# Optimization experiments

Measured on AMD Instinct MI355X. Metric: run time of the kernel, lower is better.

## Reference

```python
import jax, jax.numpy as jnp
import numpy as np

B, T, H, NH, L, V, FF = 2, 1024, 1024, 16, 6, 8192, 4096
D = H // NH
EPS = 1e-5


def _ln(x, g, b):
    mu = jnp.mean(x, axis=-1, keepdims=True)
    var = jnp.mean(jnp.square(x - mu), axis=-1, keepdims=True)
    return (x - mu) * jax.lax.rsqrt(var + EPS) * g + b


def setup_inputs() -> dict:
    key = jax.random.key(0)
    ks = jax.random.split(key, 12)
    s = 1.0 / np.sqrt(H)
    return {
        "x": jax.random.randint(ks[0], (B, T), 0, V),
        "tok_emb": jax.random.normal(ks[1], (V, H), jnp.float32) * s,
        "pos_emb": jax.random.normal(ks[2], (1, T, H), jnp.float32) * s,
        "Wq": jax.random.normal(ks[3], (L, H, H), jnp.float32) * s,
        "bq": jnp.zeros((L, H), jnp.float32),
        "Wk": jax.random.normal(ks[4], (L, H, H), jnp.float32) * s,
        "bk": jnp.zeros((L, H), jnp.float32),
        "Wv": jax.random.normal(ks[5], (L, H, H), jnp.float32) * s,
        "bv": jnp.zeros((L, H), jnp.float32),
        "Wo": jax.random.normal(ks[6], (L, H, H), jnp.float32) * s,
        "bo": jnp.zeros((L, H), jnp.float32),
        "W1": jax.random.normal(ks[7], (L, H, FF), jnp.float32) * s,
        "b1": jnp.zeros((L, FF), jnp.float32),
        "W2": jax.random.normal(ks[8], (L, FF, H), jnp.float32) * (1.0 / np.sqrt(FF)),
        "b2": jnp.zeros((L, H), jnp.float32),
        "ln1_g": jnp.ones((L, H), jnp.float32),
        "ln1_b": jnp.zeros((L, H), jnp.float32),
        "ln2_g": jnp.ones((L, H), jnp.float32),
        "ln2_b": jnp.zeros((L, H), jnp.float32),
        "lnf_g": jnp.ones((H,), jnp.float32),
        "lnf_b": jnp.zeros((H,), jnp.float32),
        "headW": jax.random.normal(ks[9], (H, V), jnp.float32) * s,
        "headb": jnp.zeros((V,), jnp.float32),
    }


def _transformer(x, tok_emb, pos_emb, Wq, bq, Wk, bk, Wv, bv, Wo, bo,
                 W1, b1, W2, b2, ln1_g, ln1_b, ln2_g, ln2_b, lnf_g, lnf_b,
                 headW, headb):
    Tcur = x.shape[1]
    h = tok_emb[x] + pos_emb[:, :Tcur, :]            # [B,T,H]
    mask = jnp.tril(jnp.ones((Tcur, Tcur), bool))    # causal [T,T]
    scale = 1.0 / np.sqrt(D)

    def block(h, p):
        (wq, q_b, wk, k_b, wv, v_b, wo, o_b,
         w1, b1_, w2, b2_, g1, be1, g2, be2) = p
        q = (h @ wq + q_b).reshape(B, Tcur, NH, D)
        k = (h @ wk + k_b).reshape(B, Tcur, NH, D)
        v = (h @ wv + v_b).reshape(B, Tcur, NH, D)
        att = jnp.einsum('bqnd,bknd->bnqk', q, k) * scale
        att = jnp.where(mask, att, -jnp.inf)
        w = jax.nn.softmax(att, axis=-1)
        o = jnp.einsum('bnqk,bknd->bqnd', w, v).reshape(B, Tcur, H)
        h = _ln(h + (o @ wo + o_b), g1, be1)          # post-LN after attention
        m = jax.nn.gelu(h @ w1 + b1_, approximate=False) @ w2 + b2_
        h = _ln(h + m, g2, be2)                       # post-LN after MLP
        return h, None

    params = (Wq, bq, Wk, bk, Wv, bv, Wo, bo, W1, b1, W2, b2,
              ln1_g, ln1_b, ln2_g, ln2_b)
    h, _ = jax.lax.scan(block, h, params)
    h = _ln(h, lnf_g, lnf_b)
    return h @ headW + headb                          # [B,T,V]


def reference(x, tok_emb, pos_emb, Wq, bq, Wk, bk, Wv, bv, Wo, bo,
              W1, b1, W2, b2, ln1_g, ln1_b, ln2_g, ln2_b, lnf_g, lnf_b,
              headW, headb):
    return _transformer(x, tok_emb, pos_emb, Wq, bq, Wk, bk, Wv, bv, Wo, bo,
                        W1, b1, W2, b2, ln1_g, ln1_b, ln2_g, ln2_b,
                        lnf_g, lnf_b, headW, headb)
```

## Files before the change

kernel.cpp:

```cpp
#include <hip/hip_runtime.h>
#include <hip/hip_bf16.h>

#define DEV __device__ __forceinline__

typedef unsigned short u16;
typedef __attribute__((ext_vector_type(8))) short bf16x8;
typedef __attribute__((ext_vector_type(4))) float f32x4;

static constexpr int MB_ = 2;
static constexpr int T_  = 1024;
static constexpr int H_  = 1024;
static constexpr int NH_ = 16;
static constexpr int L_  = 6;
static constexpr int V_  = 8192;
static constexpr int FF_ = 4096;
static constexpr int M_  = MB_ * T_;
static constexpr int QKVN = 3 * H_;

DEV u16 f2bf(float x) {
  __hip_bfloat16 h = __float2bfloat16(x);
  return *reinterpret_cast<u16*>(&h);
}
DEV float bf2f(u16 v) {
  unsigned u = (unsigned)v << 16;
  float f;
  __builtin_memcpy(&f, &u, 4);
  return f;
}

__global__ __launch_bounds__(256) void embed_concat_kernel(
    const int* __restrict__ x, const float* __restrict__ tok,
    const float* __restrict__ pos, float* __restrict__ h, u16* __restrict__ hb,
    const float* __restrict__ bq, const float* __restrict__ bk,
    const float* __restrict__ bv, float* __restrict__ outb)
{
  int i = blockIdx.x;
  if (i < M_) {
    int t = threadIdx.x;
    int id = x[i];
    int tt = i & (T_ - 1);
    float4 a = *(const float4*)(tok + (size_t)id * H_ + t * 4);
    float4 b = *(const float4*)(pos + (size_t)tt * H_ + t * 4);
    float4 r = make_float4(a.x + b.x, a.y + b.y, a.z + b.z, a.w + b.w);
    *(float4*)(h + (size_t)i * H_ + t * 4) = r;
    ushort4 u = make_ushort4(f2bf(r.x), f2bf(r.y), f2bf(r.z), f2bf(r.w));
    *(ushort4*)(hb + (size_t)i * H_ + t * 4) = u;
  } else {
    int l = i - M_;
    for (int j = threadIdx.x; j < H_; j += 256) {
      outb[(size_t)l * QKVN + j]          = bq[(size_t)l * H_ + j];
      outb[(size_t)l * QKVN + H_ + j]     = bk[(size_t)l * H_ + j];
      outb[(size_t)l * QKVN + 2 * H_ + j] = bv[(size_t)l * H_ + j];
    }
  }
}

DEV void transpose_tile128s(float (*Ts)[65], const float* __restrict__ W,
                            u16* __restrict__ WT, int R, int C, int bx, int by)
{
  const int t = threadIdx.x;
  const int lr = t >> 4;
  const int lcq = (t & 15) * 4;
  #pragma unroll
  for (int si = 0; si < 2; ++si) {
    #pragma unroll
    for (int sj = 0; sj < 2; ++sj) {
      const int r0 = by * 128 + si * 64, c0 = bx * 128 + sj * 64;
      #pragma unroll
      for (int it = 0; it < 4; ++it) {
        int r = it * 16 + lr;
        float4 v = *(const float4*)(W + (size_t)(r0 + r) * C + c0 + lcq);
        Ts[r][lcq + 0] = v.x; Ts[r][lcq + 1] = v.y;
        Ts[r][lcq + 2] = v.z; Ts[r][lcq + 3] = v.w;
      }
      __syncthreads();
      #pragma unroll
      for (int it = 0; it < 4; ++it) {
        int n = it * 16 + lr;
        ushort4 u = make_ushort4(f2bf(Ts[lcq + 0][n]), f2bf(Ts[lcq + 1][n]),
                                 f2bf(Ts[lcq + 2][n]), f2bf(Ts[lcq + 3][n]));
        *(ushort4*)(WT + (size_t)(c0 + n) * R + r0 + lcq) = u;
      }
      __syncthreads();
    }
  }
}

DEV void transpose_layer_body(float (*Ts)[65], int t,
    const float* Wq, const float* Wk, const float* Wv, const float* Wo,
    const float* W1, const float* W2,
    u16* qkvT, u16* oT, u16* w1T, u16* w2T)
{
  if (t < 256) {
    int m = t >> 6, idx = t & 63, bx = idx & 7, by = idx >> 3;
    const float* W = (m == 0) ? Wq : (m == 1) ? Wk : (m == 2) ? Wv : Wo;
    u16* WT = (m == 3) ? oT : qkvT + (size_t)m * H_ * H_;
    transpose_tile128s(Ts, W, WT, H_, H_, bx, by);
  } else if (t < 512) {
    int idx = t - 256;
    transpose_tile128s(Ts, W1, w1T, H_, FF_, idx & 31, idx >> 5);
  } else {
    int idx = t - 512;
    transpose_tile128s(Ts, W2, w2T, FF_, H_, idx & 7, idx >> 3);
  }
}

__global__ __launch_bounds__(256) void transpose_layer_k(
    const float* __restrict__ Wq, const float* __restrict__ Wk,
    const float* __restrict__ Wv, const float* __restrict__ Wo,
    const float* __restrict__ W1, const float* __restrict__ W2,
    u16* qkvT, u16* oT, u16* w1T, u16* w2T)
{
  __shared__ float Ts[64][65];
  transpose_layer_body(Ts, blockIdx.x, Wq, Wk, Wv, Wo, W1, W2, qkvT, oT, w1T, w2T);
}


#define GLOAD_LDS16(g, l)                                              \
  __builtin_amdgcn_global_load_lds(                                    \
      (const __attribute__((address_space(1))) void*)(g),              \
      (__attribute__((address_space(3))) void*)(l), 16, 0, 0)

DEV void stage_t(const u16* __restrict__ G, int ldk, int r0g, int kofs,
                 u16* lds, int w, int lane)
{
  const int rl = ((lane >> 3) << 1) | ((lane >> 2) & 1);
  #pragma unroll
  for (int j = 0; j < 2; ++j) {
    const int row0 = w * 32 + j * 16;
    const int row = row0 + rl;
    const int c = (lane & 3) ^ (((row0 >> 1) + (lane >> 3)) & 3);
    const u16* g = G + (size_t)(r0g + row) * ldk + kofs + c * 8;
    GLOAD_LDS16(g, lds + row0 * 32);
  }
}

DEV bf16x8 frag3(const u16* lds, int rr, int ch) {
  return *(const bf16x8*)(lds + (rr >> 1) * 64 + (rr & 1) * 32 +
                          ((ch ^ ((rr >> 1) & 3)) * 8));
}

template<int N>
DEV void wait_vm_barrier() {
  asm volatile("s_waitcnt vmcnt(%0)" :: "n"(N) : "memory");
  __builtin_amdgcn_s_barrier();
}

DEV void comp3(const u16* As, const u16* Bs, f32x4 (&acc)[4][4],
               int wr, int wc, int lc, int lg)
{
  bf16x8 af[4], bv[4];
  #pragma unroll
  for (int mi = 0; mi < 4; ++mi)
    af[mi] = frag3(As, wr * 64 + mi * 16 + lc, lg);
  #pragma unroll
  for (int ni = 0; ni < 4; ++ni)
    bv[ni] = frag3(Bs, wc * 64 + ni * 16 + lc, lg);
  #pragma unroll
  for (int mi = 0; mi < 4; ++mi)
    #pragma unroll
    for (int ni = 0; ni < 4; ++ni)
      acc[mi][ni] = __builtin_amdgcn_mfma_f32_16x16x32_bf16(af[mi], bv[ni], acc[mi][ni], 0, 0, 0);
}

template<bool PARTIAL, bool DO_GELU, bool WF, bool WB>
DEV void gemm_body(u16* SMEM,
    const u16* __restrict__ A, const u16* __restrict__ BT,
    const float* __restrict__ bias, float* __restrict__ Cf,
    u16* __restrict__ Cb, u16* __restrict__ Pb,
    int N, int K, int Ksub, int lid, int nwgx, int nwgy, int zid)
{
  const int tid = threadIdx.x;
  const int lane = tid & 63, w = tid >> 6;
  const int wr = w >> 1, wc = w & 1;
  const int lc = lane & 15, lg = lane >> 4;

  const int nwg = nwgx * nwgy;
  const int q8 = nwg >> 3, r8s = nwg & 7;
  const int xcd = lid & 7, ord = lid >> 3;
  const int sid = (xcd < r8s ? xcd * (q8 + 1) : r8s * (q8 + 1) + (xcd - r8s) * q8) + ord;
  const int m0 = (sid % nwgy) * 128, n0 = (sid / nwgy) * 128;

  const int kb = zid * Ksub;
  const int NT = Ksub >> 5;

  f32x4 acc[4][4];
  #pragma unroll
  for (int i = 0; i < 4; ++i)
    #pragma unroll
    for (int j = 0; j < 4; ++j) {
      f32x4 z = {0.f, 0.f, 0.f, 0.f};
      acc[i][j] = z;
    }

  auto STG = [&](int t, int b) {
    stage_t(A,  K, m0, kb + t * 32, SMEM + b * 4096, w, lane);
    stage_t(BT, K, n0, kb + t * 32, SMEM + 16384 + b * 4096, w, lane);
  };

  STG(0, 0);
  STG(1, 1);
  int t = 0;
  for (; t < NT - 2; ++t) {
    STG(t + 2, (t + 2) & 3);
    wait_vm_barrier<8>();
    comp3(SMEM + (t & 3) * 4096, SMEM + 16384 + (t & 3) * 4096, acc, wr, wc, lc, lg);
  }
  wait_vm_barrier<4>();
  comp3(SMEM + (t & 3) * 4096, SMEM + 16384 + (t & 3) * 4096, acc, wr, wc, lc, lg);
  ++t;
  wait_vm_barrier<0>();
  comp3(SMEM + (t & 3) * 4096, SMEM + 16384 + (t & 3) * 4096, acc, wr, wc, lc, lg);

  const size_t zofs = (size_t)zid * M_ * N;
  #pragma unroll
  for (int mi = 0; mi < 4; ++mi) {
    #pragma unroll
    for (int ni = 0; ni < 4; ++ni) {
      int gn = n0 + wc * 64 + ni * 16 + lc;
      float bvv = PARTIAL ? 0.f : bias[gn];
      #pragma unroll
      for (int r = 0; r < 4; ++r) {
        int gm = m0 + wr * 64 + mi * 16 + lg * 4 + r;
        float v = acc[mi][ni][r];
        if (PARTIAL) {
          Pb[zofs + (size_t)gm * N + gn] = f2bf(v);
        } else {
          v += bvv;
          if (DO_GELU) v = 0.5f * v * (1.f + erff(v * 0.70710678118654752f));
          if (WF) Cf[(size_t)gm * N + gn] = v;
          if (WB) Cb[(size_t)gm * N + gn] = f2bf(v);
        }
      }
    }
  }
}

template<bool PARTIAL, bool DO_GELU, bool WF, bool WB>
__global__ __launch_bounds__(256, 2) void gemm3(
    const u16* __restrict__ A, const u16* __restrict__ BT,
    const float* __restrict__ bias, float* __restrict__ Cf,
    u16* __restrict__ Cb, u16* __restrict__ Pb, int N, int K, int Ksub)
{
  __shared__ __align__(16) u16 SMEM[32768];
  gemm_body<PARTIAL, DO_GELU, WF, WB>(SMEM, A, BT, bias, Cf, Cb, Pb, N, K, Ksub,
      blockIdx.y * gridDim.x + blockIdx.x, gridDim.x, gridDim.y, blockIdx.z);
}

__global__ __launch_bounds__(256, 2) void gemmW1_fused(
    const u16* __restrict__ A, const u16* __restrict__ w1T,
    const float* __restrict__ bias, u16* __restrict__ m1,
    const float* nWq, const float* nWk, const float* nWv, const float* nWo,
    const float* nW1, const float* nW2,
    u16* nqkvT, u16* noT, u16* nw1T, u16* nw2T,
    const float* hW, u16* hT)
{
  __shared__ __align__(16) u16 SMEM[32768];
  const int id = blockIdx.x;
  if (id < 512) {
    gemm_body<false, true, false, true>(SMEM, A, w1T, bias, nullptr, m1, nullptr,
                                        FF_, H_, H_, id, 32, 16, 0);
  } else if (nWq) {
    float (*Ts)[65] = (float(*)[65])SMEM;
    transpose_layer_body(Ts, id - 512, nWq, nWk, nWv, nWo, nW1, nW2,
                         nqkvT, noT, nw1T, nw2T);
  } else {
    float (*Ts)[65] = (float(*)[65])SMEM;
    int idx = id - 512;
    transpose_tile128s(Ts, hW, hT, H_, V_, idx & 63, idx >> 6);
  }
}

__global__ __launch_bounds__(256) void ln2_kernel(
    const u16* __restrict__ Pb, int S,
    const float* __restrict__ bias,
    const float* __restrict__ g, const float* __restrict__ be,
    const float* __restrict__ gf, const float* __restrict__ bef,
    float* __restrict__ h, u16* __restrict__ hb)
{
  __shared__ float red[8];
  int row = blockIdx.x, t = threadIdx.x;
  int lane = t & 63, w = t >> 6;
  float4 v = *(const float4*)(h + (size_t)row * H_ + t * 4);
  float4 bb = *(const float4*)(bias + t * 4);
  v.x += bb.x; v.y += bb.y; v.z += bb.z; v.w += bb.w;
  for (int s0 = 0; s0 < S; ++s0) {
    ushort4 p = *(const ushort4*)(Pb + (size_t)s0 * M_ * H_ + (size_t)row * H_ + t * 4);
    v.x += bf2f(p.x); v.y += bf2f(p.y); v.z += bf2f(p.z); v.w += bf2f(p.w);
  }
  float s = v.x + v.y + v.z + v.w;
  float q = v.x * v.x + v.y * v.y + v.z * v.z + v.w * v.w;
  #pragma unroll
  for (int o = 1; o < 64; o <<= 1) { s += __shfl_xor(s, o); q += __shfl_xor(q, o); }
  if (lane == 0) { red[w] = s; red[4 + w] = q; }
  __syncthreads();
  float S1 = red[0] + red[1] + red[2] + red[3];
  float Q1 = red[4] + red[5] + red[6] + red[7];
  float mu  = S1 * (1.f / H_);
  float var = Q1 * (1.f / H_) - mu * mu;
  float inv = rsqrtf(var + 1e-5f);
  float4 gv = *(const float4*)(g  + t * 4);
  float4 bv = *(const float4*)(be + t * 4);
  float o0 = (v.x - mu) * inv * gv.x + bv.x;
  float o1 = (v.y - mu) * inv * gv.y + bv.y;
  float o2 = (v.z - mu) * inv * gv.z + bv.z;
  float o3 = (v.w - mu) * inv * gv.w + bv.w;
  if (gf == nullptr) {
    *(float4*)(h + (size_t)row * H_ + t * 4) = make_float4(o0, o1, o2, o3);
    ushort4 u = make_ushort4(f2bf(o0), f2bf(o1), f2bf(o2), f2bf(o3));
    *(ushort4*)(hb + (size_t)row * H_ + t * 4) = u;
  } else {
    float s2 = o0 + o1 + o2 + o3;
    float q2 = o0 * o0 + o1 * o1 + o2 * o2 + o3 * o3;
    #pragma unroll
    for (int o = 1; o < 64; o <<= 1) { s2 += __shfl_xor(s2, o); q2 += __shfl_xor(q2, o); }
    __syncthreads();
    if (lane == 0) { red[w] = s2; red[4 + w] = q2; }
    __syncthreads();
    float S2 = red[0] + red[1] + red[2] + red[3];
    float Q2 = red[4] + red[5] + red[6] + red[7];
    float mu2  = S2 * (1.f / H_);
    float var2 = Q2 * (1.f / H_) - mu2 * mu2;
    float inv2 = rsqrtf(var2 + 1e-5f);
    float4 gv2 = *(const float4*)(gf  + t * 4);
    float4 bv2 = *(const float4*)(bef + t * 4);
    ushort4 u = make_ushort4(f2bf((o0 - mu2) * inv2 * gv2.x + bv2.x),
                             f2bf((o1 - mu2) * inv2 * gv2.y + bv2.y),
                             f2bf((o2 - mu2) * inv2 * gv2.z + bv2.z),
                             f2bf((o3 - mu2) * inv2 * gv2.w + bv2.w));
    *(ushort4*)(hb + (size_t)row * H_ + t * 4) = u;
  }
}

__global__ __launch_bounds__(256) void attn_kernel(
    const u16* __restrict__ qkv, u16* __restrict__ Og)
{
  __shared__ __align__(16) u16 Ks[2][64][72];
  __shared__ __align__(16) u16 Vs[2][64][72];
  __shared__ __align__(16) u16 QPs[4][16][72];

  const int qb = gridDim.x - 1 - blockIdx.x;
  const int bh = blockIdx.y;
  const int b = bh >> 4, hh = bh & 15;
  const int q0 = qb * 64;
  const size_t base  = ((size_t)b * T_) * QKVN + (size_t)hh * 64;
  const size_t baseO = ((size_t)b * T_) * H_ + (size_t)hh * 64;

  const int tid = threadIdx.x;
  const int lane = tid & 63, w = tid >> 6;
  const int lc = lane & 15, lg = lane >> 4;

  const int r8 = tid >> 3, d8 = (tid & 7) << 3;
  const int vk = tid & 31, vd = (tid >> 5) << 3;

  u16* Qflat = &QPs[0][0][0];

  bf16x8 kr[2], vr[2];
  #pragma unroll
  for (int i = 0; i < 2; ++i) {
    kr[i] = *(const bf16x8*)(qkv + base + H_ + (size_t)(i * 32 + r8) * QKVN + d8);
    vr[i] = *(const bf16x8*)(qkv + base + 2 * H_ + (size_t)(i * 32 + vk) * QKVN + vd);
  }
  #pragma unroll
  for (int i = 0; i < 2; ++i)
    *(bf16x8*)(Qflat + (size_t)(i * 32 + r8) * 72 + d8) =
      *(const bf16x8*)(qkv + base + (size_t)(q0 + i * 32 + r8) * QKVN + d8);
  #pragma unroll
  for (int i = 0; i < 2; ++i) {
    *(bf16x8*)&Ks[0][i * 32 + r8][d8] = kr[i];
    #pragma unroll
    for (int j = 0; j < 8; ++j) Vs[0][vd + j][i * 32 + vk] = ((const u16*)&vr[i])[j];
  }
  __syncthreads();
  bf16x8 aq0 = *(const bf16x8*)(Qflat + (size_t)(w * 16 + lc) * 72 + lg * 8);
  bf16x8 aq1 = *(const bf16x8*)(Qflat + (size_t)(w * 16 + lc) * 72 + 32 + lg * 8);

  float m_r[4], l_r[4];
  f32x4 oa[4];
  #pragma unroll
  for (int i = 0; i < 4; ++i) {
    m_r[i] = -1e30f; l_r[i] = 0.f;
    f32x4 z = {0.f, 0.f, 0.f, 0.f};
    oa[i] = z;
  }
  const float sc2 = 0.125f * 1.4426950408889634f;

  for (int kv = 0; kv <= qb; ++kv) {
    const int cur = kv & 1, nxt = cur ^ 1;
    if (kv < qb) {
      #pragma unroll
      for (int i = 0; i < 2; ++i) {
        kr[i] = *(const bf16x8*)(qkv + base + H_ + (size_t)((kv + 1) * 64 + i * 32 + r8) * QKVN + d8);
        vr[i] = *(const bf16x8*)(qkv + base + 2 * H_ + (size_t)((kv + 1) * 64 + i * 32 + vk) * QKVN + vd);
      }
    }

    f32x4 sfr[4];
    #pragma unroll
    for (int ni = 0; ni < 4; ++ni) { f32x4 z = {0.f,0.f,0.f,0.f}; sfr[ni] = z; }
    __builtin_amdgcn_s_setprio(1);
    #pragma unroll
    for (int ni = 0; ni < 4; ++ni) {
      bf16x8 bk0 = *(const bf16x8*)&Ks[cur][ni * 16 + lc][lg * 8];
      bf16x8 bk1 = *(const bf16x8*)&Ks[cur][ni * 16 + lc][32 + lg * 8];
      sfr[ni] = __builtin_amdgcn_mfma_f32_16x16x32_bf16(aq0, bk0, sfr[ni], 0, 0, 0);
      sfr[ni] = __builtin_amdgcn_mfma_f32_16x16x32_bf16(aq1, bk1, sfr[ni], 0, 0, 0);
    }
    __builtin_amdgcn_s_setprio(0);
    if (kv == qb) {
      #pragma unroll
      for (int ni = 0; ni < 4; ++ni)
        #pragma unroll
        for (int r = 0; r < 4; ++r)
          if (ni * 16 + lc > w * 16 + lg * 4 + r) sfr[ni][r] = -1e30f;
    }
    #pragma unroll
    for (int r = 0; r < 4; ++r) {
      float pm = fmaxf(fmaxf(sfr[0][r], sfr[1][r]), fmaxf(sfr[2][r], sfr[3][r]));
      pm = fmaxf(pm, __shfl_xor(pm, 1));
      pm = fmaxf(pm, __shfl_xor(pm, 2));
      pm = fmaxf(pm, __shfl_xor(pm, 4));
      pm = fmaxf(pm, __shfl_xor(pm, 8));
      float mn = fmaxf(m_r[r], pm);
      float al = exp2f(sc2 * (m_r[r] - mn));
      m_r[r] = mn; l_r[r] *= al;
      #pragma unroll
      for (int f = 0; f < 4; ++f) oa[f][r] *= al;
      float rs = 0.f;
      #pragma unroll
      for (int ni = 0; ni < 4; ++ni) {
        float p = exp2f(sc2 * (sfr[ni][r] - mn));
        sfr[ni][r] = p; rs += p;
      }
      rs += __shfl_xor(rs, 1); rs += __shfl_xor(rs, 2);
      rs += __shfl_xor(rs, 4); rs += __shfl_xor(rs, 8);
      l_r[r] += rs;
    }
    #pragma unroll
    for (int ni = 0; ni < 4; ++ni)
      #pragma unroll
      for (int r = 0; r < 4; ++r)
        QPs[w][lg * 4 + r][ni * 16 + lc] = f2bf(sfr[ni][r]);
    bf16x8 ap0 = *(const bf16x8*)&QPs[w][lc][lg * 8];
    bf16x8 ap1 = *(const bf16x8*)&QPs[w][lc][32 + lg * 8];
    __builtin_amdgcn_s_setprio(1);
    #pragma unroll
    for (int f = 0; f < 4; ++f) {
      bf16x8 bv0 = *(const bf16x8*)&Vs[cur][f * 16 + lc][lg * 8];
      bf16x8 bv1 = *(const bf16x8*)&Vs[cur][f * 16 + lc][32 + lg * 8];
      oa[f] = __builtin_amdgcn_mfma_f32_16x16x32_bf16(ap0, bv0, oa[f], 0, 0, 0);
      oa[f] = __builtin_amdgcn_mfma_f32_16x16x32_bf16(ap1, bv1, oa[f], 0, 0, 0);
    }
    __builtin_amdgcn_s_setprio(0);

    if (kv < qb) {
      #pragma unroll
      for (int i = 0; i < 2; ++i) {
        *(bf16x8*)&Ks[nxt][i * 32 + r8][d8] = kr[i];
        #pragma unroll
        for (int j = 0; j < 8; ++j) Vs[nxt][vd + j][i * 32 + vk] = ((const u16*)&vr[i])[j];
      }
      __syncthreads();
    }
  }

  #pragma unroll
  for (int r = 0; r < 4; ++r) {
    float inv = 1.f / l_r[r];
    int grow = q0 + w * 16 + lg * 4 + r;
    #pragma unroll
    for (int f = 0; f < 4; ++f)
      Og[baseO + (size_t)grow * H_ + f * 16 + lc] = f2bf(oa[f][r] * inv);
  }
}

extern "C" void kernel_launch(void* const* d_in, const int* in_sizes, int n_in,
                              void* d_out, int out_size, void* d_ws, size_t ws_size,
                              hipStream_t stream)
{
  const int*   x    = (const int*)  d_in[0];
  const float* tok  = (const float*)d_in[1];
  const float* pos  = (const float*)d_in[2];
  const float* Wq   = (const float*)d_in[3];
  const float* bq   = (const float*)d_in[4];
  const float* Wk   = (const float*)d_in[5];
  const float* bk   = (const float*)d_in[6];
  const float* Wv   = (const float*)d_in[7];
  const float* bv   = (const float*)d_in[8];
  const float* Wo   = (const float*)d_in[9];
  const float* bo   = (const float*)d_in[10];
  const float* W1   = (const float*)d_in[11];
  const float* b1   = (const float*)d_in[12];
  const float* W2   = (const float*)d_in[13];
  const float* b2   = (const float*)d_in[14];
  const float* g1   = (const float*)d_in[15];
  const float* be1  = (const float*)d_in[16];
  const float* g2   = (const float*)d_in[17];
  const float* be2  = (const float*)d_in[18];
  const float* gf   = (const float*)d_in[19];
  const float* bef  = (const float*)d_in[20];
  const float* hW   = (const float*)d_in[21];
  const float* hbias= (const float*)d_in[22];
  float* out = (float*)d_out;

  char* wsp = (char*)d_ws;
  size_t off = 0;
  auto alloc = [&](size_t bytes) -> void* {
    void* p = wsp + off;
    off += (bytes + 255) & ~(size_t)255;
    return p;
  };
  float* h    = (float*)alloc((size_t)M_ * H_ * 4);
  u16*   hb   = (u16*)  alloc((size_t)M_ * H_ * 2);
  u16*   qkv  = (u16*)  alloc((size_t)M_ * QKVN * 2);
  u16*   ob_  = (u16*)  alloc((size_t)M_ * H_ * 2);
  u16*   m1   = (u16*)  alloc((size_t)M_ * FF_ * 2);
  u16*   Pb   = (u16*)  alloc((size_t)4 * M_ * H_ * 2);
  u16*   hT   = (u16*)  alloc((size_t)V_ * H_ * 2);
  u16*   qkvT = (u16*)  alloc((size_t)QKVN * H_ * 2);
  u16*   oT   = (u16*)  alloc((size_t)H_ * H_ * 2);
  u16*   w1Tb = (u16*)  alloc((size_t)2 * H_ * FF_ * 2);
  u16*   w2Tb = (u16*)  alloc((size_t)2 * FF_ * H_ * 2);
  float* bqkv = (float*)alloc((size_t)L_ * QKVN * 4);
  (void)in_sizes; (void)n_in; (void)out_size; (void)ws_size;

  auto w1T = [&](int l) { return w1Tb + (size_t)(l & 1) * H_ * FF_; };
  auto w2T = [&](int l) { return w2Tb + (size_t)(l & 1) * FF_ * H_; };

  embed_concat_kernel<<<M_ + L_, 256, 0, stream>>>(x, tok, pos, h, hb,
                                                   bq, bk, bv, bqkv);
  transpose_layer_k<<<768, 256, 0, stream>>>(
      Wq, Wk, Wv, Wo, W1, W2, qkvT, oT, w1T(0), w2T(0));

  for (int l = 0; l < L_; ++l) {
    gemm3<false, false, false, true><<<dim3(QKVN / 128, M_ / 128, 1), 256, 0, stream>>>(
        hb, qkvT, bqkv + (size_t)l * QKVN, nullptr, qkv, nullptr, QKVN, H_, H_);
    attn_kernel<<<dim3(T_ / 64, MB_ * NH_), 256, 0, stream>>>(qkv, ob_);
    gemm3<true, false, false, false><<<dim3(H_ / 128, M_ / 128, 4), 256, 0, stream>>>(
        ob_, oT, nullptr, nullptr, nullptr, Pb, H_, H_, H_ / 4);
    ln2_kernel<<<M_, 256, 0, stream>>>(Pb, 4, bo + l * H_, g1 + l * H_, be1 + l * H_,
                                       nullptr, nullptr, h, hb);
    if (l + 1 < L_) {
      int nl = l + 1;
      gemmW1_fused<<<512 + 768, 256, 0, stream>>>(
          hb, w1T(l), b1 + (size_t)l * FF_, m1,
          Wq + (size_t)nl * H_ * H_, Wk + (size_t)nl * H_ * H_,
          Wv + (size_t)nl * H_ * H_, Wo + (size_t)nl * H_ * H_,
          W1 + (size_t)nl * H_ * FF_, W2 + (size_t)nl * FF_ * H_,
          qkvT, oT, w1T(nl), w2T(nl), nullptr, nullptr);
    } else {
      gemmW1_fused<<<512 + 512, 256, 0, stream>>>(
          hb, w1T(l), b1 + (size_t)l * FF_, m1,
          nullptr, nullptr, nullptr, nullptr, nullptr, nullptr,
          nullptr, nullptr, nullptr, nullptr, hW, hT);
    }
    gemm3<true, false, false, false><<<dim3(H_ / 128, M_ / 128, 4), 256, 0, stream>>>(
        m1, w2T(l), nullptr, nullptr, nullptr, Pb, H_, FF_, FF_ / 4);
    if (l + 1 < L_) {
      ln2_kernel<<<M_, 256, 0, stream>>>(Pb, 4, b2 + l * H_, g2 + l * H_, be2 + l * H_,
                                         nullptr, nullptr, h, hb);
    } else {
      ln2_kernel<<<M_, 256, 0, stream>>>(Pb, 4, b2 + l * H_, g2 + l * H_, be2 + l * H_,
                                         gf, bef, h, hb);
    }
  }

  gemm3<false, false, true, false><<<dim3(V_ / 128, M_ / 128, 1), 256, 0, stream>>>(
      hb, hT, hbias, out, nullptr, nullptr, V_, H_, H_);
}
```

Measured before the change: 1.006 ms.

## Widen GEMM tiles to 128x256 with 512-thread workgroups and dynamic LDS

Replaces the 128x128, 256-thread GEMM kernel with a 128x256 tile computed by 8 waves (2x4 wave grid), staging B with twice as many rows per k-step into a larger 4-stage ring held in 96KB of dynamic shared memory. The goal is more reuse of each A tile per staged byte and fewer workgroups per GEMM. The fused W1 kernel and its weight-transpose side work now run at 512 threads, with the upper half of threads idle during transposes. Risks: one workgroup per CU lowers occupancy, and the grids get smaller, so some GEMMs (for example the split-K ones with 128 workgroups) may underfill the GPU.

New measurement: 1.020 ms. No clear change (+1.4%).

```diff
diff --git a/kernel.cpp b/kernel.cpp
--- a/kernel.cpp
+++ b/kernel.cpp
@@ -16,6 +16,7 @@
 static constexpr int FF_ = 4096;
 static constexpr int M_  = MB_ * T_;
 static constexpr int QKVN = 3 * H_;
+static constexpr size_t GLDS = 98304;
 
 DEV u16 f2bf(float x) {
   __hip_bfloat16 h = __float2bfloat16(x);
@@ -59,27 +60,32 @@
                             u16* __restrict__ WT, int R, int C, int bx, int by)
 {
   const int t = threadIdx.x;
-  const int lr = t >> 4;
+  const bool act = t < 256;
+  const int lr = (t & 255) >> 4;
   const int lcq = (t & 15) * 4;
   #pragma unroll
   for (int si = 0; si < 2; ++si) {
     #pragma unroll
     for (int sj = 0; sj < 2; ++sj) {
       const int r0 = by * 128 + si * 64, c0 = bx * 128 + sj * 64;
-      #pragma unroll
-      for (int it = 0; it < 4; ++it) {
-        int r = it * 16 + lr;
-        float4 v = *(const float4*)(W + (size_t)(r0 + r) * C + c0 + lcq);
-        Ts[r][lcq + 0] = v.x; Ts[r][lcq + 1] = v.y;
-        Ts[r][lcq + 2] = v.z; Ts[r][lcq + 3] = v.w;
+      if (act) {
+        #pragma unroll
+        for (int it = 0; it < 4; ++it) {
+          int r = it * 16 + lr;
+          float4 v = *(const float4*)(W + (size_t)(r0 + r) * C + c0 + lcq);
+          Ts[r][lcq + 0] = v.x; Ts[r][lcq + 1] = v.y;
+          Ts[r][lcq + 2] = v.z; Ts[r][lcq + 3] = v.w;
+        }
       }
       __syncthreads();
-      #pragma unroll
-      for (int it = 0; it < 4; ++it) {
-        int n = it * 16 + lr;
-        ushort4 u = make_ushort4(f2bf(Ts[lcq + 0][n]), f2bf(Ts[lcq + 1][n]),
-                                 f2bf(Ts[lcq + 2][n]), f2bf(Ts[lcq + 3][n]));
-        *(ushort4*)(WT + (size_t)(c0 + n) * R + r0 + lcq) = u;
+      if (act) {
+        #pragma unroll
+        for (int it = 0; it < 4; ++it) {
+          int n = it * 16 + lr;
+          ushort4 u = make_ushort4(f2bf(Ts[lcq + 0][n]), f2bf(Ts[lcq + 1][n]),
+                                   f2bf(Ts[lcq + 2][n]), f2bf(Ts[lcq + 3][n]));
+          *(ushort4*)(WT + (size_t)(c0 + n) * R + r0 + lcq) = u;
+        }
       }
       __syncthreads();
     }
@@ -121,18 +127,14 @@
       (const __attribute__((address_space(1))) void*)(g),              \
       (__attribute__((address_space(3))) void*)(l), 16, 0, 0)
 
-DEV void stage_t(const u16* __restrict__ G, int ldk, int r0g, int kofs,
-                 u16* lds, int w, int lane)
+DEV void stage_rows16(const u16* __restrict__ G, int ldk, int r0g, int row0,
+                      int kofs, u16* lds, int lane)
 {
   const int rl = ((lane >> 3) << 1) | ((lane >> 2) & 1);
-  #pragma unroll
-  for (int j = 0; j < 2; ++j) {
-    const int row0 = w * 32 + j * 16;
-    const int row = row0 + rl;
-    const int c = (lane & 3) ^ (((row0 >> 1) + (lane >> 3)) & 3);
-    const u16* g = G + (size_t)(r0g + row) * ldk + kofs + c * 8;
-    GLOAD_LDS16(g, lds + row0 * 32);
-  }
+  const int row = row0 + rl;
+  const int c = (lane & 3) ^ (((row0 >> 1) + (lane >> 3)) & 3);
+  const u16* g = G + (size_t)(r0g + row) * ldk + kofs + c * 8;
+  GLOAD_LDS16(g, lds + row0 * 32);
 }
 
 DEV bf16x8 frag3(const u16* lds, int rr, int ch) {
@@ -146,16 +148,16 @@
   __builtin_amdgcn_s_barrier();
 }
 
-DEV void comp3(const u16* As, const u16* Bs, f32x4 (&acc)[4][4],
-               int wr, int wc, int lc, int lg)
+DEV void comp8(const u16* As, const u16* Bs, f32x4 (&acc)[4][4],
+               int wm, int wn, int lc, int lg)
 {
   bf16x8 af[4], bv[4];
   #pragma unroll
   for (int mi = 0; mi < 4; ++mi)
-    af[mi] = frag3(As, wr * 64 + mi * 16 + lc, lg);
+    af[mi] = frag3(As, wm * 64 + mi * 16 + lc, lg);
   #pragma unroll
   for (int ni = 0; ni < 4; ++ni)
-    bv[ni] = frag3(Bs, wc * 64 + ni * 16 + lc, lg);
+    bv[ni] = frag3(Bs, wn * 64 + ni * 16 + lc, lg);
   #pragma unroll
   for (int mi = 0; mi < 4; ++mi)
     #pragma unroll
@@ -164,7 +166,7 @@
 }
 
 template<bool PARTIAL, bool DO_GELU, bool WF, bool WB>
-DEV void gemm_body(u16* SMEM,
+DEV void gemm8_body(u16* SMEM,
     const u16* __restrict__ A, const u16* __restrict__ BT,
     const float* __restrict__ bias, float* __restrict__ Cf,
     u16* __restrict__ Cb, u16* __restrict__ Pb,
@@ -172,14 +174,14 @@
 {
   const int tid = threadIdx.x;
   const int lane = tid & 63, w = tid >> 6;
-  const int wr = w >> 1, wc = w & 1;
+  const int wm = w >> 2, wn = w & 3;
   const int lc = lane & 15, lg = lane >> 4;
 
   const int nwg = nwgx * nwgy;
   const int q8 = nwg >> 3, r8s = nwg & 7;
   const int xcd = lid & 7, ord = lid >> 3;
   const int sid = (xcd < r8s ? xcd * (q8 + 1) : r8s * (q8 + 1) + (xcd - r8s) * q8) + ord;
-  const int m0 = (sid % nwgy) * 128, n0 = (sid / nwgy) * 128;
+  const int m0 = (sid % nwgy) * 128, n0 = (sid / nwgy) * 256;
 
   const int kb = zid * Ksub;
   const int NT = Ksub >> 5;
@@ -194,8 +196,9 @@
     }
 
   auto STG = [&](int t, int b) {
-    stage_t(A,  K, m0, kb + t * 32, SMEM + b * 4096, w, lane);
-    stage_t(BT, K, n0, kb + t * 32, SMEM + 16384 + b * 4096, w, lane);
+    stage_rows16(A,  K, m0, w * 16,      kb + t * 32, SMEM + b * 4096, lane);
+    stage_rows16(BT, K, n0, w * 32,      kb + t * 32, SMEM + 16384 + b * 8192, lane);
+    stage_rows16(BT, K, n0, w * 32 + 16, kb + t * 32, SMEM + 16384 + b * 8192, lane);
   };
 
   STG(0, 0);
@@ -203,25 +206,25 @@
   int t = 0;
   for (; t < NT - 2; ++t) {
     STG(t + 2, (t + 2) & 3);
-    wait_vm_barrier<8>();
-    comp3(SMEM + (t & 3) * 4096, SMEM + 16384 + (t & 3) * 4096, acc, wr, wc, lc, lg);
-  }
-  wait_vm_barrier<4>();
-  comp3(SMEM + (t & 3) * 4096, SMEM + 16384 + (t & 3) * 4096, acc, wr, wc, lc, lg);
+    wait_vm_barrier<6>();
+    comp8(SMEM + (t & 3) * 4096, SMEM + 16384 + (t & 3) * 8192, acc, wm, wn, lc, lg);
+  }
+  wait_vm_barrier<3>();
+  comp8(SMEM + (t & 3) * 4096, SMEM + 16384 + (t & 3) * 8192, acc, wm, wn, lc, lg);
   ++t;
   wait_vm_barrier<0>();
-  comp3(SMEM + (t & 3) * 4096, SMEM + 16384 + (t & 3) * 4096, acc, wr, wc, lc, lg);
+  comp8(SMEM + (t & 3) * 4096, SMEM + 16384 + (t & 3) * 8192, acc, wm, wn, lc, lg);
 
   const size_t zofs = (size_t)zid * M_ * N;
   #pragma unroll
   for (int mi = 0; mi < 4; ++mi) {
     #pragma unroll
     for (int ni = 0; ni < 4; ++ni) {
-      int gn = n0 + wc * 64 + ni * 16 + lc;
+      int gn = n0 + wn * 64 + ni * 16 + lc;
       float bvv = PARTIAL ? 0.f : bias[gn];
       #pragma unroll
       for (int r = 0; r < 4; ++r) {
-        int gm = m0 + wr * 64 + mi * 16 + lg * 4 + r;
+        int gm = m0 + wm * 64 + mi * 16 + lg * 4 + r;
         float v = acc[mi][ni][r];
         if (PARTIAL) {
           Pb[zofs + (size_t)gm * N + gn] = f2bf(v);
@@ -237,17 +240,17 @@
 }
 
 template<bool PARTIAL, bool DO_GELU, bool WF, bool WB>
-__global__ __launch_bounds__(256, 2) void gemm3(
+__global__ __launch_bounds__(512, 1) void gemm8(
     const u16* __restrict__ A, const u16* __restrict__ BT,
     const float* __restrict__ bias, float* __restrict__ Cf,
     u16* __restrict__ Cb, u16* __restrict__ Pb, int N, int K, int Ksub)
 {
-  __shared__ __align__(16) u16 SMEM[32768];
-  gemm_body<PARTIAL, DO_GELU, WF, WB>(SMEM, A, BT, bias, Cf, Cb, Pb, N, K, Ksub,
+  extern __shared__ __align__(16) u16 SMEM[];
+  gemm8_body<PARTIAL, DO_GELU, WF, WB>(SMEM, A, BT, bias, Cf, Cb, Pb, N, K, Ksub,
       blockIdx.y * gridDim.x + blockIdx.x, gridDim.x, gridDim.y, blockIdx.z);
 }
 
-__global__ __launch_bounds__(256, 2) void gemmW1_fused(
+__global__ __launch_bounds__(512, 1) void gemmW1_fused(
     const u16* __restrict__ A, const u16* __restrict__ w1T,
     const float* __restrict__ bias, u16* __restrict__ m1,
     const float* nWq, const float* nWk, const float* nWv, const float* nWo,
@@ -255,18 +258,18 @@
     u16* nqkvT, u16* noT, u16* nw1T, u16* nw2T,
     const float* hW, u16* hT)
 {
-  __shared__ __align__(16) u16 SMEM[32768];
+  extern __shared__ __align__(16) u16 SMEM[];
   const int id = blockIdx.x;
-  if (id < 512) {
-    gemm_body<false, true, false, true>(SMEM, A, w1T, bias, nullptr, m1, nullptr,
-                                        FF_, H_, H_, id, 32, 16, 0);
+  if (id < 256) {
+    gemm8_body<false, true, false, true>(SMEM, A, w1T, bias, nullptr, m1, nullptr,
+                                         FF_, H_, H_, id, 16, 16, 0);
   } else if (nWq) {
     float (*Ts)[65] = (float(*)[65])SMEM;
-    transpose_layer_body(Ts, id - 512, nWq, nWk, nWv, nWo, nW1, nW2,
+    transpose_layer_body(Ts, id - 256, nWq, nWk, nWv, nWo, nW1, nW2,
                          nqkvT, noT, nw1T, nw2T);
   } else {
     float (*Ts)[65] = (float(*)[65])SMEM;
-    int idx = id - 512;
+    int idx = id - 256;
     transpose_tile128s(Ts, hW, hT, H_, V_, idx & 63, idx >> 6);
   }
 }
@@ -533,28 +536,28 @@
       Wq, Wk, Wv, Wo, W1, W2, qkvT, oT, w1T(0), w2T(0));
 
   for (int l = 0; l < L_; ++l) {
-    gemm3<false, false, false, true><<<dim3(QKVN / 128, M_ / 128, 1), 256, 0, stream>>>(
+    gemm8<false, false, false, true><<<dim3(QKVN / 256, M_ / 128, 1), 512, GLDS, stream>>>(
         hb, qkvT, bqkv + (size_t)l * QKVN, nullptr, qkv, nullptr, QKVN, H_, H_);
     attn_kernel<<<dim3(T_ / 64, MB_ * NH_), 256, 0, stream>>>(qkv, ob_);
-    gemm3<true, false, false, false><<<dim3(H_ / 128, M_ / 128, 4), 256, 0, stream>>>(
+    gemm8<true, false, false, false><<<dim3(H_ / 256, M_ / 128, 4), 512, GLDS, stream>>>(
         ob_, oT, nullptr, nullptr, nullptr, Pb, H_, H_, H_ / 4);
     ln2_kernel<<<M_, 256, 0, stream>>>(Pb, 4, bo + l * H_, g1 + l * H_, be1 + l * H_,
                                        nullptr, nullptr, h, hb);
     if (l + 1 < L_) {
       int nl = l + 1;
-      gemmW1_fused<<<512 + 768, 256, 0, stream>>>(
+      gemmW1_fused<<<256 + 768, 512, GLDS, stream>>>(
           hb, w1T(l), b1 + (size_t)l * FF_, m1,
           Wq + (size_t)nl * H_ * H_, Wk + (size_t)nl * H_ * H_,
           Wv + (size_t)nl * H_ * H_, Wo + (size_t)nl * H_ * H_,
           W1 + (size_t)nl * H_ * FF_, W2 + (size_t)nl * FF_ * H_,
           qkvT, oT, w1T(nl), w2T(nl), nullptr, nullptr);
     } else {
-      gemmW1_fused<<<512 + 512, 256, 0, stream>>>(
+      gemmW1_fused<<<256 + 512, 512, GLDS, stream>>>(
           hb, w1T(l), b1 + (size_t)l * FF_, m1,
           nullptr, nullptr, nullptr, nullptr, nullptr, nullptr,
           nullptr, nullptr, nullptr, nullptr, hW, hT);
     }
-    gemm3<true, false, false, false><<<dim3(H_ / 128, M_ / 128, 4), 256, 0, stream>>>(
+    gemm8<true, false, false, false><<<dim3(H_ / 256, M_ / 128, 4), 512, GLDS, stream>>>(
         m1, w2T(l), nullptr, nullptr, nullptr, Pb, H_, FF_, FF_ / 4);
     if (l + 1 < L_) {
       ln2_kernel<<<M_, 256, 0, stream>>>(Pb, 4, b2 + l * H_, g2 + l * H_, be2 + l * H_,
@@ -565,6 +568,6 @@
     }
   }
 
-  gemm3<false, false, true, false><<<dim3(V_ / 128, M_ / 128, 1), 256, 0, stream>>>(
+  gemm8<false, false, true, false><<<dim3(V_ / 256, M_ / 128, 1), 512, GLDS, stream>>>(
       hb, hT, hbias, out, nullptr, nullptr, V_, H_, H_);
 }
```

## Enlarge attention query tile to 128 rows with 8 warps sharing K/V tiles

Applied to the files above, without the earlier changes.

The attention kernel now processes 128 query rows per block with 512 threads (8 wavefronts), so each staged 64-row K/V tile in shared memory is reused by twice as many query rows. Each wavefront skips K/V tiles that lie entirely above its causal diagonal and masks only the partially covered tile. This halves the grid size and the K/V global loads per query row, but creates intra-block imbalance near the diagonal, since idle wavefronts still wait at barriers, and gives fewer blocks to fill the GPU.

Result: no change. 994.9 us (-1.1%).

```diff
diff --git a/kernel.cpp b/kernel.cpp
--- a/kernel.cpp
+++ b/kernel.cpp
@@ -332,17 +332,17 @@
   }
 }
 
-__global__ __launch_bounds__(256) void attn_kernel(
+__global__ __launch_bounds__(512) void attn_kernel(
     const u16* __restrict__ qkv, u16* __restrict__ Og)
 {
   __shared__ __align__(16) u16 Ks[2][64][72];
   __shared__ __align__(16) u16 Vs[2][64][72];
-  __shared__ __align__(16) u16 QPs[4][16][72];
+  __shared__ __align__(16) u16 QPs[8][16][72];
 
   const int qb = gridDim.x - 1 - blockIdx.x;
   const int bh = blockIdx.y;
   const int b = bh >> 4, hh = bh & 15;
-  const int q0 = qb * 64;
+  const int q0 = qb * 128;
   const size_t base  = ((size_t)b * T_) * QKVN + (size_t)hh * 64;
   const size_t baseO = ((size_t)b * T_) * H_ + (size_t)hh * 64;
 
@@ -350,30 +350,23 @@
   const int lane = tid & 63, w = tid >> 6;
   const int lc = lane & 15, lg = lane >> 4;
 
-  const int r8 = tid >> 3, d8 = (tid & 7) << 3;
-  const int vk = tid & 31, vd = (tid >> 5) << 3;
-
-  u16* Qflat = &QPs[0][0][0];
-
-  bf16x8 kr[2], vr[2];
-  #pragma unroll
-  for (int i = 0; i < 2; ++i) {
-    kr[i] = *(const bf16x8*)(qkv + base + H_ + (size_t)(i * 32 + r8) * QKVN + d8);
-    vr[i] = *(const bf16x8*)(qkv + base + 2 * H_ + (size_t)(i * 32 + vk) * QKVN + vd);
-  }
-  #pragma unroll
-  for (int i = 0; i < 2; ++i)
-    *(bf16x8*)(Qflat + (size_t)(i * 32 + r8) * 72 + d8) =
-      *(const bf16x8*)(qkv + base + (size_t)(q0 + i * 32 + r8) * QKVN + d8);
-  #pragma unroll
-  for (int i = 0; i < 2; ++i) {
-    *(bf16x8*)&Ks[0][i * 32 + r8][d8] = kr[i];
-    #pragma unroll
-    for (int j = 0; j < 8; ++j) Vs[0][vd + j][i * 32 + vk] = ((const u16*)&vr[i])[j];
-  }
+  const int rk = tid >> 3, dk = (tid & 7) << 3;
+  const int vk = tid & 63, vd = (tid >> 6) << 3;
+  const int rq = tid >> 2, cq = (tid & 3) << 4;
+
+  bf16x8 kr, vr;
+  kr = *(const bf16x8*)(qkv + base + H_ + (size_t)rk * QKVN + dk);
+  vr = *(const bf16x8*)(qkv + base + 2 * H_ + (size_t)vk * QKVN + vd);
+  *(bf16x8*)&QPs[rq >> 4][rq & 15][cq] =
+      *(const bf16x8*)(qkv + base + (size_t)(q0 + rq) * QKVN + cq);
+  *(bf16x8*)&QPs[rq >> 4][rq & 15][cq + 8] =
+      *(const bf16x8*)(qkv + base + (size_t)(q0 + rq) * QKVN + cq + 8);
+  *(bf16x8*)&Ks[0][rk][dk] = kr;
+  #pragma unroll
+  for (int j = 0; j < 8; ++j) Vs[0][vd + j][vk] = ((const u16*)&vr)[j];
   __syncthreads();
-  bf16x8 aq0 = *(const bf16x8*)(Qflat + (size_t)(w * 16 + lc) * 72 + lg * 8);
-  bf16x8 aq1 = *(const bf16x8*)(Qflat + (size_t)(w * 16 + lc) * 72 + 32 + lg * 8);
+  bf16x8 aq0 = *(const bf16x8*)&QPs[w][lc][lg * 8];
+  bf16x8 aq1 = *(const bf16x8*)&QPs[w][lc][32 + lg * 8];
 
   float m_r[4], l_r[4];
   f32x4 oa[4];
@@ -384,82 +377,82 @@
     oa[i] = z;
   }
   const float sc2 = 0.125f * 1.4426950408889634f;
-
-  for (int kv = 0; kv <= qb; ++kv) {
+  const int NT = 2 * qb + 2;
+  const int rmin = q0 + w * 16;
+
+  for (int kv = 0; kv < NT; ++kv) {
     const int cur = kv & 1, nxt = cur ^ 1;
-    if (kv < qb) {
-      #pragma unroll
-      for (int i = 0; i < 2; ++i) {
-        kr[i] = *(const bf16x8*)(qkv + base + H_ + (size_t)((kv + 1) * 64 + i * 32 + r8) * QKVN + d8);
-        vr[i] = *(const bf16x8*)(qkv + base + 2 * H_ + (size_t)((kv + 1) * 64 + i * 32 + vk) * QKVN + vd);
-      }
-    }
-
-    f32x4 sfr[4];
-    #pragma unroll
-    for (int ni = 0; ni < 4; ++ni) { f32x4 z = {0.f,0.f,0.f,0.f}; sfr[ni] = z; }
-    __builtin_amdgcn_s_setprio(1);
-    #pragma unroll
-    for (int ni = 0; ni < 4; ++ni) {
-      bf16x8 bk0 = *(const bf16x8*)&Ks[cur][ni * 16 + lc][lg * 8];
-      bf16x8 bk1 = *(const bf16x8*)&Ks[cur][ni * 16 + lc][32 + lg * 8];
-      sfr[ni] = __builtin_amdgcn_mfma_f32_16x16x32_bf16(aq0, bk0, sfr[ni], 0, 0, 0);
-      sfr[ni] = __builtin_amdgcn_mfma_f32_16x16x32_bf16(aq1, bk1, sfr[ni], 0, 0, 0);
-    }
-    __builtin_amdgcn_s_setprio(0);
-    if (kv == qb) {
+    if (kv + 1 < NT) {
+      kr = *(const bf16x8*)(qkv + base + H_ + (size_t)((kv + 1) * 64 + rk) * QKVN + dk);
+      vr = *(const bf16x8*)(qkv + base + 2 * H_ + (size_t)((kv + 1) * 64 + vk) * QKVN + vd);
+    }
+
+    const bool live = (kv * 64 <= rmin + 15);
+    if (live) {
+      const bool partial = (kv * 64 + 63 > rmin);
+      f32x4 sfr[4];
+      #pragma unroll
+      for (int ni = 0; ni < 4; ++ni) { f32x4 z = {0.f,0.f,0.f,0.f}; sfr[ni] = z; }
+      __builtin_amdgcn_s_setprio(1);
+      #pragma unroll
+      for (int ni = 0; ni < 4; ++ni) {
+        bf16x8 bk0 = *(const bf16x8*)&Ks[cur][ni * 16 + lc][lg * 8];
+        bf16x8 bk1 = *(const bf16x8*)&Ks[cur][ni * 16 + lc][32 + lg * 8];
+        sfr[ni] = __builtin_amdgcn_mfma_f32_16x16x32_bf16(aq0, bk0, sfr[ni], 0, 0, 0);
+        sfr[ni] = __builtin_amdgcn_mfma_f32_16x16x32_bf16(aq1, bk1, sfr[ni], 0, 0, 0);
+      }
+      __builtin_amdgcn_s_setprio(0);
+      if (partial) {
+        #pragma unroll
+        for (int ni = 0; ni < 4; ++ni)
+          #pragma unroll
+          for (int r = 0; r < 4; ++r)
+            if (kv * 64 + ni * 16 + lc > rmin + lg * 4 + r) sfr[ni][r] = -1e30f;
+      }
+      #pragma unroll
+      for (int r = 0; r < 4; ++r) {
+        float pm = fmaxf(fmaxf(sfr[0][r], sfr[1][r]), fmaxf(sfr[2][r], sfr[3][r]));
+        pm = fmaxf(pm, __shfl_xor(pm, 1));
+        pm = fmaxf(pm, __shfl_xor(pm, 2));
+        pm = fmaxf(pm, __shfl_xor(pm, 4));
+        pm = fmaxf(pm, __shfl_xor(pm, 8));
+        float mn = fmaxf(m_r[r], pm);
+        float al = exp2f(sc2 * (m_r[r] - mn));
+        m_r[r] = mn; l_r[r] *= al;
+        #pragma unroll
+        for (int f = 0; f < 4; ++f) oa[f][r] *= al;
+        float rs = 0.f;
+        #pragma unroll
+        for (int ni = 0; ni < 4; ++ni) {
+          float p = exp2f(sc2 * (sfr[ni][r] - mn));
+          sfr[ni][r] = p; rs += p;
+        }
+        rs += __shfl_xor(rs, 1); rs += __shfl_xor(rs, 2);
+        rs += __shfl_xor(rs, 4); rs += __shfl_xor(rs, 8);
+        l_r[r] += rs;
+      }
       #pragma unroll
       for (int ni = 0; ni < 4; ++ni)
         #pragma unroll
         for (int r = 0; r < 4; ++r)
-          if (ni * 16 + lc > w * 16 + lg * 4 + r) sfr[ni][r] = -1e30f;
-    }
-    #pragma unroll
-    for (int r = 0; r < 4; ++r) {
-      float pm = fmaxf(fmaxf(sfr[0][r], sfr[1][r]), fmaxf(sfr[2][r], sfr[3][r]));
-      pm = fmaxf(pm, __shfl_xor(pm, 1));
-      pm = fmaxf(pm, __shfl_xor(pm, 2));
-      pm = fmaxf(pm, __shfl_xor(pm, 4));
-      pm = fmaxf(pm, __shfl_xor(pm, 8));
-      float mn = fmaxf(m_r[r], pm);
-      float al = exp2f(sc2 * (m_r[r] - mn));
-      m_r[r] = mn; l_r[r] *= al;
-      #pragma unroll
-      for (int f = 0; f < 4; ++f) oa[f][r] *= al;
-      float rs = 0.f;
-      #pragma unroll
-      for (int ni = 0; ni < 4; ++ni) {
-        float p = exp2f(sc2 * (sfr[ni][r] - mn));
-        sfr[ni][r] = p; rs += p;
-      }
-      rs += __shfl_xor(rs, 1); rs += __shfl_xor(rs, 2);
-      rs += __shfl_xor(rs, 4); rs += __shfl_xor(rs, 8);
-      l_r[r] += rs;
-    }
-    #pragma unroll
-    for (int ni = 0; ni < 4; ++ni)
-      #pragma unroll
-      for (int r = 0; r < 4; ++r)
-        QPs[w][lg * 4 + r][ni * 16 + lc] = f2bf(sfr[ni][r]);
-    bf16x8 ap0 = *(const bf16x8*)&QPs[w][lc][lg * 8];
-    bf16x8 ap1 = *(const bf16x8*)&QPs[w][lc][32 + lg * 8];
-    __builtin_amdgcn_s_setprio(1);
-    #pragma unroll
-    for (int f = 0; f < 4; ++f) {
-      bf16x8 bv0 = *(const bf16x8*)&Vs[cur][f * 16 + lc][lg * 8];
-      bf16x8 bv1 = *(const bf16x8*)&Vs[cur][f * 16 + lc][32 + lg * 8];
-      oa[f] = __builtin_amdgcn_mfma_f32_16x16x32_bf16(ap0, bv0, oa[f], 0, 0, 0);
-      oa[f] = __builtin_amdgcn_mfma_f32_16x16x32_bf16(ap1, bv1, oa[f], 0, 0, 0);
-    }
-    __builtin_amdgcn_s_setprio(0);
-
-    if (kv < qb) {
-      #pragma unroll
-      for (int i = 0; i < 2; ++i) {
-        *(bf16x8*)&Ks[nxt][i * 32 + r8][d8] = kr[i];
-        #pragma unroll
-        for (int j = 0; j < 8; ++j) Vs[nxt][vd + j][i * 32 + vk] = ((const u16*)&vr[i])[j];
-      }
+          QPs[w][lg * 4 + r][ni * 16 + lc] = f2bf(sfr[ni][r]);
+      bf16x8 ap0 = *(const bf16x8*)&QPs[w][lc][lg * 8];
+      bf16x8 ap1 = *(const bf16x8*)&QPs[w][lc][32 + lg * 8];
+      __builtin_amdgcn_s_setprio(1);
+      #pragma unroll
+      for (int f = 0; f < 4; ++f) {
+        bf16x8 bv0 = *(const bf16x8*)&Vs[cur][f * 16 + lc][lg * 8];
+        bf16x8 bv1 = *(const bf16x8*)&Vs[cur][f * 16 + lc][32 + lg * 8];
+        oa[f] = __builtin_amdgcn_mfma_f32_16x16x32_bf16(ap0, bv0, oa[f], 0, 0, 0);
+        oa[f] = __builtin_amdgcn_mfma_f32_16x16x32_bf16(ap1, bv1, oa[f], 0, 0, 0);
+      }
+      __builtin_amdgcn_s_setprio(0);
+    }
+
+    if (kv + 1 < NT) {
+      *(bf16x8*)&Ks[nxt][rk][dk] = kr;
+      #pragma unroll
+      for (int j = 0; j < 8; ++j) Vs[nxt][vd + j][vk] = ((const u16*)&vr)[j];
       __syncthreads();
     }
   }
@@ -535,7 +528,7 @@
   for (int l = 0; l < L_; ++l) {
     gemm3<false, false, false, true><<<dim3(QKVN / 128, M_ / 128, 1), 256, 0, stream>>>(
         hb, qkvT, bqkv + (size_t)l * QKVN, nullptr, qkv, nullptr, QKVN, H_, H_);
-    attn_kernel<<<dim3(T_ / 64, MB_ * NH_), 256, 0, stream>>>(qkv, ob_);
+    attn_kernel<<<dim3(T_ / 128, MB_ * NH_), 512, 0, stream>>>(qkv, ob_);
     gemm3<true, false, false, false><<<dim3(H_ / 128, M_ / 128, 4), 256, 0, stream>>>(
         ob_, oT, nullptr, nullptr, nullptr, Pb, H_, H_, H_ / 4);
     ln2_kernel<<<M_, 256, 0, stream>>>(Pb, 4, bo + l * H_, g1 + l * H_, be1 + l * H_,
```
